# Kernel optimization log

Measured on AMD Instinct MI355X. Metric: run time of the kernel, lower is better.

The kernel has to match this reference:

```python
import jax, jax.numpy as jnp
import numpy as np
from jax import lax

HEADS = 8
LN_EPS = 1e-5


def setup_inputs() -> dict:
    key = jax.random.key(0)
    k = jax.random.split(key, 8)
    B, C, H, W, r = 4, 64, 64, 64, 4
    T = H * W
    x = jax.random.normal(k[0], (B, C, H, W), dtype=jnp.float32)
    conv_w = jax.random.normal(k[1], (C, C, r, r), dtype=jnp.float32) * 0.02  # OIHW
    conv_b = jnp.zeros((C,), dtype=jnp.float32)
    ln_g = jnp.ones((C,), dtype=jnp.float32)
    ln_b = jnp.zeros((C,), dtype=jnp.float32)
    Wqkv = jax.random.normal(k[2], (C, 3 * C), dtype=jnp.float32) * 0.02  # to_qvk (no bias)
    W0 = jax.random.normal(k[3], (C, C), dtype=jnp.float32) * 0.02  # output proj (no bias)
    E = jax.random.normal(k[4], (T, T // 4), dtype=jnp.float32)  # Linformer proj (randn in torch fwd)
    return {"x": x, "conv_w": conv_w, "conv_b": conv_b, "ln_g": ln_g,
            "ln_b": ln_b, "Wqkv": Wqkv, "W0": W0, "E": E}


def _layernorm2d(y, g, b):
    # LayerNorm over channel dim of NCHW (torch: permute to NHWC, LN last dim)
    yt = y.transpose(0, 2, 3, 1)  # b h w c
    mu = yt.mean(-1, keepdims=True)
    var = ((yt - mu) ** 2).mean(-1, keepdims=True)
    yt = (yt - mu) * lax.rsqrt(var + LN_EPS) * g + b
    return yt.transpose(0, 3, 1, 2)


def reference(x, conv_w, conv_b, ln_g, ln_b, Wqkv, W0, E):
    B, C, H, W = x.shape
    T = H * W
    dh = C // HEADS
    r = conv_w.shape[-1]

    # reducer: conv(stride=r) + LayerNorm2d. NOTE: faithful to the torch module,
    # this result is computed but NEVER used by the output (dead code in source).
    red = lax.conv_general_dilated(x, conv_w, (r, r), 'VALID',
                                   dimension_numbers=('NCHW', 'OIHW', 'NCHW'))
    red = red + conv_b[None, :, None, None]
    _red = _layernorm2d(red, ln_g, ln_b)  # unused, matches source

    # tokens from full-resolution x: b c h w -> b (h w) c
    xf = x.reshape(B, C, T).transpose(0, 2, 1)  # [B,T,C]
    qkv = xf @ Wqkv  # [B,T,3C]
    # rearrange 'b t (d k h)' with k=3, h=HEADS -> composite order (d, k, h)
    qkv = qkv.reshape(B, T, dh, 3, HEADS)
    q = qkv[:, :, :, 0, :].transpose(0, 3, 1, 2)  # [B,h,T,d]
    kk = qkv[:, :, :, 1, :].transpose(0, 3, 1, 2)
    v = qkv[:, :, :, 2, :].transpose(0, 3, 1, 2)

    # Linformer low-rank projection of V and K: [B,h,T,d] x [T,k] -> [B,h,k,d]
    v = jnp.einsum('bhjd,jk->bhkd', v, E)
    kk = jnp.einsum('bhjd,jk->bhkd', kk, E)

    scale = dh ** -0.5
    scores = jnp.einsum('bhid,bhjd->bhij', q, kk) * scale  # [B,h,T,k]
    attn = jax.nn.softmax(scores, axis=-1)
    out = jnp.einsum('bhij,bhjd->bhid', attn, v)  # [B,h,T,d]

    out = out.transpose(0, 2, 1, 3).reshape(B, T, C)  # b h i d -> b i (h d)
    out = out @ W0  # [B,T,C]
    return out.transpose(0, 2, 1).reshape(B, C, H, W)
```

## Files before the change

kernel.cpp:

```cpp
#include <hip/hip_runtime.h>

#define T_DIM 4096
#define KD    1024
#define SCALE 0.35355339059327373f

typedef __attribute__((ext_vector_type(8))) short bf16x8;
typedef __attribute__((ext_vector_type(4))) short bf16x4;
typedef __attribute__((ext_vector_type(4))) float f32x4;

__device__ inline unsigned cvt_pk_bf16(float a, float b) {
  unsigned ua = __float_as_uint(a); ua += 0x7fffu + ((ua >> 16) & 1u);
  unsigned ub = __float_as_uint(b); ub += 0x7fffu + ((ub >> 16) & 1u);
  return (ua >> 16) | (ub & 0xffff0000u);
}

__device__ inline bf16x4 mk4(unsigned lo, unsigned hi) {
  union { unsigned u[2]; bf16x4 v; } x; x.u[0] = lo; x.u[1] = hi; return x.v;
}

__device__ inline bf16x8 mk8(unsigned a, unsigned b, unsigned c, unsigned d) {
  union { unsigned u[4]; bf16x8 v; } x;
  x.u[0] = a; x.u[1] = b; x.u[2] = c; x.u[3] = d; return x.v;
}

__device__ inline f32x4 mfma16(bf16x4 a, bf16x4 b, f32x4 c) {
  bf16x8 a8 = {}, b8 = {};
  a8[0] = a[0]; a8[1] = a[1]; a8[2] = a[2]; a8[3] = a[3];
  b8[0] = b[0]; b8[1] = b[1]; b8[2] = b[2]; b8[3] = b[3];
  return __builtin_amdgcn_mfma_f32_16x16x32_bf16(a8, b8, c, 0, 0, 0);
}

__global__ __launch_bounds__(256) void k_q(const float* __restrict__ x,
                                           const float* __restrict__ Wqkv,
                                           float* __restrict__ Q) {
  const int g  = blockIdx.x;
  const int tt = blockIdx.y;
  const int b  = blockIdx.z;
  const int t  = tt * 256 + threadIdx.x;
  const int col0 = g * 24;

  float acc[8];
#pragma unroll
  for (int j = 0; j < 8; ++j) acc[j] = 0.f;

  const float* xb = x + (size_t)b * 64 * T_DIM + t;
#pragma unroll 4
  for (int c = 0; c < 64; ++c) {
    float xv = xb[(size_t)c * T_DIM];
    const float* wr = Wqkv + c * 192 + col0;
#pragma unroll
    for (int h = 0; h < 8; ++h) acc[h] += xv * wr[h];
  }
#pragma unroll
  for (int h = 0; h < 8; ++h)
    Q[(((size_t)(b * 8 + h)) * 8 + g) * T_DIM + t] = acc[h];
}

__global__ __launch_bounds__(256) void k_xe(const float* __restrict__ x,
                                            const float* __restrict__ E,
                                            float* __restrict__ partial) {
  __shared__ unsigned short As[64 * 72];
  const int kb = blockIdx.x;
  const int b  = blockIdx.y;
  const int s  = blockIdx.z;
  const int k0 = kb * 128;
  const int tid = threadIdx.x;
  const int lane = tid & 63;
  const int w = tid >> 6;
  const int li = lane & 15, lg = lane >> 4;

  f32x4 acc[4][2] = {};

  const int ar = tid >> 4;
  const int af = tid & 15;

  for (int tb = 0; tb < 4; ++tb) {
    const int t0 = s * 256 + tb * 64;
    float4 av[4];
#pragma unroll
    for (int ii = 0; ii < 4; ++ii)
      av[ii] = *(const float4*)(x + ((size_t)b * 64 + ar + ii * 16) * T_DIM + t0 + af * 4);
    __syncthreads();
#pragma unroll
    for (int ii = 0; ii < 4; ++ii) {
      unsigned lo = cvt_pk_bf16(av[ii].x, av[ii].y);
      unsigned hi = cvt_pk_bf16(av[ii].z, av[ii].w);
      *(uint2*)(As + (ar + ii * 16) * 72 + af * 4) = make_uint2(lo, hi);
    }
    __syncthreads();

#pragma unroll
    for (int ks = 0; ks < 2; ++ks) {
      const int tbase = t0 + ks * 32 + lg * 8;
      bf16x8 bq[2];
#pragma unroll
      for (int nt = 0; nt < 2; ++nt) {
        const int kcol = k0 + w * 32 + nt * 16 + li;
        float bv[8];
#pragma unroll
        for (int j = 0; j < 8; ++j)
          bv[j] = E[(size_t)(tbase + j) * KD + kcol];
        bq[nt] = mk8(cvt_pk_bf16(bv[0], bv[1]), cvt_pk_bf16(bv[2], bv[3]),
                     cvt_pk_bf16(bv[4], bv[5]), cvt_pk_bf16(bv[6], bv[7]));
      }
#pragma unroll
      for (int mt = 0; mt < 4; ++mt) {
        bf16x8 af8 = *(const bf16x8*)(As + (mt * 16 + li) * 72 + ks * 32 + lg * 8);
#pragma unroll
        for (int nt = 0; nt < 2; ++nt)
          acc[mt][nt] = __builtin_amdgcn_mfma_f32_16x16x32_bf16(af8, bq[nt], acc[mt][nt], 0, 0, 0);
      }
    }
  }

  float* pb = partial + ((size_t)s * 4 + b) * (64 * KD);
#pragma unroll
  for (int mt = 0; mt < 4; ++mt)
#pragma unroll
    for (int nt = 0; nt < 2; ++nt) {
      const int row = mt * 16 + lg * 4;
      const int col = k0 + w * 32 + nt * 16 + li;
#pragma unroll
      for (int reg = 0; reg < 4; ++reg)
        pb[(size_t)(row + reg) * KD + col] = acc[mt][nt][reg];
    }
}

__global__ __launch_bounds__(256) void k_xered(const float* __restrict__ partial,
                                               unsigned short* __restrict__ XP) {
  const size_t o = ((size_t)blockIdx.x * 256 + threadIdx.x) * 4;
  const int k4 = (int)(o & 1023);
  const int cb = (int)(o >> 10);
  const size_t src = (size_t)cb * KD + k4;
  float4 a = make_float4(0.f, 0.f, 0.f, 0.f);
#pragma unroll
  for (int s = 0; s < 16; ++s) {
    float4 v = *(const float4*)(partial + ((size_t)s * 4) * (64 * KD) + src);
    a.x += v.x; a.y += v.y; a.z += v.z; a.w += v.w;
  }
  *(uint2*)(XP + o) = make_uint2(cvt_pk_bf16(a.x, a.y), cvt_pk_bf16(a.z, a.w));
}

__global__ __launch_bounds__(256) void k_kvp(const unsigned short* __restrict__ XP,
                                             const float* __restrict__ Wqkv,
                                             float* __restrict__ KVP) {
  const int kb  = blockIdx.x >> 1;
  const int sel = blockIdx.x & 1;
  const int h   = blockIdx.y;
  const int b   = blockIdx.z;
  const int k   = kb * 256 + threadIdx.x;

  float acc[8];
#pragma unroll
  for (int d = 0; d < 8; ++d) acc[d] = 0.f;

  const unsigned short* xb = XP + (size_t)b * 64 * KD + k;
#pragma unroll 4
  for (int c = 0; c < 64; ++c) {
    float xv = __uint_as_float((unsigned)xb[(size_t)c * KD] << 16);
    const float* wr = Wqkv + c * 192 + (sel + 1) * 8 + h;
#pragma unroll
    for (int d = 0; d < 8; ++d) acc[d] += xv * wr[d * 24];
  }

  float* op = KVP + (((size_t)(b * 8 + h)) * KD + k) * 16 + sel * 8;
  *(float4*)(op)     = make_float4(acc[0], acc[1], acc[2], acc[3]);
  *(float4*)(op + 4) = make_float4(acc[4], acc[5], acc[6], acc[7]);
}

#define VT_PITCH 1032
__global__ __launch_bounds__(256) void k_attn(const float* __restrict__ Q,
                                              const float* __restrict__ KVP,
                                              float* __restrict__ O) {
  __shared__ unsigned short Kt[2 * 1024 * 4];
  __shared__ unsigned short Vt[9 * VT_PITCH];
  const int bh = blockIdx.x;
  const int tid = threadIdx.x;
  const float ks = SCALE;

#pragma unroll
  for (int it = 0; it < 4; ++it) {
    const int j = it * 256 + tid;
    const float* row = KVP + ((size_t)bh * 1024 + j) * 16;
    float4 k0 = *(const float4*)(row);
    float4 k1 = *(const float4*)(row + 4);
    float4 v0 = *(const float4*)(row + 8);
    float4 v1 = *(const float4*)(row + 12);
    unsigned a0 = cvt_pk_bf16(k0.x * ks, k0.y * ks);
    unsigned a1 = cvt_pk_bf16(k0.z * ks, k0.w * ks);
    unsigned a2 = cvt_pk_bf16(k1.x * ks, k1.y * ks);
    unsigned a3 = cvt_pk_bf16(k1.z * ks, k1.w * ks);
    *(uint2*)(&Kt[(size_t)j * 4])          = make_uint2(a0, a1);
    *(uint2*)(&Kt[(size_t)(1024 + j) * 4]) = make_uint2(a2, a3);
    unsigned b0 = cvt_pk_bf16(v0.x, v0.y);
    unsigned b1 = cvt_pk_bf16(v0.z, v0.w);
    unsigned b2 = cvt_pk_bf16(v1.x, v1.y);
    unsigned b3 = cvt_pk_bf16(v1.z, v1.w);
    Vt[0 * VT_PITCH + j] = (unsigned short)b0;
    Vt[1 * VT_PITCH + j] = (unsigned short)(b0 >> 16);
    Vt[2 * VT_PITCH + j] = (unsigned short)b1;
    Vt[3 * VT_PITCH + j] = (unsigned short)(b1 >> 16);
    Vt[4 * VT_PITCH + j] = (unsigned short)b2;
    Vt[5 * VT_PITCH + j] = (unsigned short)(b2 >> 16);
    Vt[6 * VT_PITCH + j] = (unsigned short)b3;
    Vt[7 * VT_PITCH + j] = (unsigned short)(b3 >> 16);
    Vt[8 * VT_PITCH + j] = 0x3F80;
  }
  __syncthreads();

  const int lane = tid & 63, w = tid >> 6;
  const int li = lane & 15, lg = lane >> 4;
  const int i0w = blockIdx.y * 128 + w * 32;

  bf16x4 qf[2] = {bf16x4{}, bf16x4{}};
  if (lane < 32) {
#pragma unroll
    for (int it2 = 0; it2 < 2; ++it2) {
      const float* qp = Q + ((size_t)bh * 8 + lg * 4) * T_DIM + i0w + it2 * 16 + li;
      qf[it2] = mk4(cvt_pk_bf16(qp[0], qp[T_DIM]),
                    cvt_pk_bf16(qp[2 * T_DIM], qp[3 * T_DIM]));
    }
  }

  f32x4 accO[2] = {f32x4{0.f, 0.f, 0.f, 0.f}, f32x4{0.f, 0.f, 0.f, 0.f}};
#pragma unroll 2
  for (int jt = 0; jt < 1024; jt += 16) {
    bf16x4 kf = {};
    if (lane < 32) kf = *(const bf16x4*)(&Kt[(size_t)(lg * 1024 + jt + li) * 4]);
    bf16x4 vf = {};
    if (li < 9) vf = *(const bf16x4*)(&Vt[li * VT_PITCH + jt + lg * 4]);
#pragma unroll
    for (int it2 = 0; it2 < 2; ++it2) {
      f32x4 st = mfma16(kf, qf[it2], f32x4{0.f, 0.f, 0.f, 0.f});
      f32x4 p;
      p[0] = __expf(st[0]); p[1] = __expf(st[1]);
      p[2] = __expf(st[2]); p[3] = __expf(st[3]);
      bf16x4 pf = mk4(cvt_pk_bf16(p[0], p[1]), cvt_pk_bf16(p[2], p[3]));
      accO[it2] = mfma16(vf, pf, accO[it2]);
    }
  }

  const int b = bh >> 3, h = bh & 7;
#pragma unroll
  for (int it2 = 0; it2 < 2; ++it2) {
    float l = __shfl(accO[it2][0], 32 + li);
    float inv = 1.0f / l;
    if (lane < 32) {
      const int i = i0w + it2 * 16 + li;
      float4 o = make_float4(accO[it2][0] * inv, accO[it2][1] * inv,
                             accO[it2][2] * inv, accO[it2][3] * inv);
      *(float4*)(O + ((size_t)b * T_DIM + i) * 64 + h * 8 + lg * 4) = o;
    }
  }
}

__global__ __launch_bounds__(256) void k_out(const float* __restrict__ O,
                                             const float* __restrict__ W0,
                                             float* __restrict__ out) {
  const int cg = blockIdx.x;
  const int tt = blockIdx.y;
  const int b  = blockIdx.z;
  const int t  = tt * 256 + threadIdx.x;
  const int col0 = cg * 8;

  float acc[8];
#pragma unroll
  for (int j = 0; j < 8; ++j) acc[j] = 0.f;

  const float* orow = O + ((size_t)b * T_DIM + t) * 64;
#pragma unroll
  for (int c0 = 0; c0 < 64; c0 += 4) {
    float4 v = *(const float4*)(orow + c0);
    float ov[4] = {v.x, v.y, v.z, v.w};
#pragma unroll
    for (int u = 0; u < 4; ++u) {
      const float* wr = W0 + (c0 + u) * 64 + col0;
#pragma unroll
      for (int j = 0; j < 8; ++j) acc[j] += ov[u] * wr[j];
    }
  }
#pragma unroll
  for (int j = 0; j < 8; ++j)
    out[((size_t)b * 64 + col0 + j) * T_DIM + t] = acc[j];
}

extern "C" void kernel_launch(void* const* d_in, const int* in_sizes, int n_in,
                              void* d_out, int out_size, void* d_ws, size_t ws_size,
                              hipStream_t stream) {
  const float* x    = (const float*)d_in[0];
  const float* Wqkv = (const float*)d_in[5];
  const float* W0   = (const float*)d_in[6];
  const float* E    = (const float*)d_in[7];
  float* out = (float*)d_out;

  float* Q       = (float*)d_ws;
  float* O       = Q + 1048576;
  float* KVP     = O + 1048576;
  float* partial = KVP + 524288;
  unsigned short* XP = (unsigned short*)(partial + 4194304);

  k_q     <<<dim3(8, 16, 4), 256, 0, stream>>>(x, Wqkv, Q);
  k_xe    <<<dim3(8, 4, 16), 256, 0, stream>>>(x, E, partial);
  k_xered <<<dim3(256),      256, 0, stream>>>(partial + (size_t)0, XP);
  k_kvp   <<<dim3(8, 8, 4),  256, 0, stream>>>(XP, Wqkv, KVP);
  k_attn  <<<dim3(32, 32),   256, 0, stream>>>(Q, KVP, O);
  k_out   <<<dim3(8, 16, 4), 256, 0, stream>>>(O, W0, out);
}
```

Baseline: 167.9 us.

## Precompute scaled bf16 K/V layouts in k_kvp and drop LDS staging in k_xe

k_kvp now writes K already scaled and packed as bf16 in the layout the attention kernel's shared memory expects, and V as transposed bf16 rows. k_attn therefore only copies these into LDS, with no fp32 loads or per-block conversion. This matters because each of the 32 blocks per head previously re-read and re-converted the same fp32 KVP. k_xe also drops its shared-memory staging of x and its barriers, loading x fragments straight from global into MFMA operands, which trades fewer syncs for more redundant global reads across waves.

```diff
diff --git a/kernel.cpp b/kernel.cpp
--- a/kernel.cpp
+++ b/kernel.cpp
@@ -7,6 +7,12 @@
 typedef __attribute__((ext_vector_type(8))) short bf16x8;
 typedef __attribute__((ext_vector_type(4))) short bf16x4;
 typedef __attribute__((ext_vector_type(4))) float f32x4;
+
+__device__ inline unsigned short f2bf(float f) {
+  unsigned u = __float_as_uint(f);
+  unsigned r = u + 0x7fffu + ((u >> 16) & 1u);
+  return (unsigned short)(r >> 16);
+}
 
 __device__ inline unsigned cvt_pk_bf16(float a, float b) {
   unsigned ua = __float_as_uint(a); ua += 0x7fffu + ((ua >> 16) & 1u);
@@ -59,7 +65,6 @@
 __global__ __launch_bounds__(256) void k_xe(const float* __restrict__ x,
                                             const float* __restrict__ E,
                                             float* __restrict__ partial) {
-  __shared__ unsigned short As[64 * 72];
   const int kb = blockIdx.x;
   const int b  = blockIdx.y;
   const int s  = blockIdx.z;
@@ -71,45 +76,29 @@
 
   f32x4 acc[4][2] = {};
 
-  const int ar = tid >> 4;
-  const int af = tid & 15;
-
-  for (int tb = 0; tb < 4; ++tb) {
-    const int t0 = s * 256 + tb * 64;
-    float4 av[4];
-#pragma unroll
-    for (int ii = 0; ii < 4; ++ii)
-      av[ii] = *(const float4*)(x + ((size_t)b * 64 + ar + ii * 16) * T_DIM + t0 + af * 4);
-    __syncthreads();
-#pragma unroll
-    for (int ii = 0; ii < 4; ++ii) {
-      unsigned lo = cvt_pk_bf16(av[ii].x, av[ii].y);
-      unsigned hi = cvt_pk_bf16(av[ii].z, av[ii].w);
-      *(uint2*)(As + (ar + ii * 16) * 72 + af * 4) = make_uint2(lo, hi);
-    }
-    __syncthreads();
-
-#pragma unroll
-    for (int ks = 0; ks < 2; ++ks) {
-      const int tbase = t0 + ks * 32 + lg * 8;
-      bf16x8 bq[2];
-#pragma unroll
-      for (int nt = 0; nt < 2; ++nt) {
-        const int kcol = k0 + w * 32 + nt * 16 + li;
-        float bv[8];
-#pragma unroll
-        for (int j = 0; j < 8; ++j)
-          bv[j] = E[(size_t)(tbase + j) * KD + kcol];
-        bq[nt] = mk8(cvt_pk_bf16(bv[0], bv[1]), cvt_pk_bf16(bv[2], bv[3]),
-                     cvt_pk_bf16(bv[4], bv[5]), cvt_pk_bf16(bv[6], bv[7]));
-      }
-#pragma unroll
-      for (int mt = 0; mt < 4; ++mt) {
-        bf16x8 af8 = *(const bf16x8*)(As + (mt * 16 + li) * 72 + ks * 32 + lg * 8);
-#pragma unroll
-        for (int nt = 0; nt < 2; ++nt)
-          acc[mt][nt] = __builtin_amdgcn_mfma_f32_16x16x32_bf16(af8, bq[nt], acc[mt][nt], 0, 0, 0);
-      }
+#pragma unroll 2
+  for (int tb = 0; tb < 8; ++tb) {
+    const int tbase = s * 256 + tb * 32 + lg * 8;
+    bf16x8 bq[2];
+#pragma unroll
+    for (int nt = 0; nt < 2; ++nt) {
+      const int kcol = k0 + w * 32 + nt * 16 + li;
+      float bv[8];
+#pragma unroll
+      for (int j = 0; j < 8; ++j)
+        bv[j] = E[(size_t)(tbase + j) * KD + kcol];
+      bq[nt] = mk8(cvt_pk_bf16(bv[0], bv[1]), cvt_pk_bf16(bv[2], bv[3]),
+                   cvt_pk_bf16(bv[4], bv[5]), cvt_pk_bf16(bv[6], bv[7]));
+    }
+#pragma unroll
+    for (int mt = 0; mt < 4; ++mt) {
+      const float* ap = x + ((size_t)b * 64 + mt * 16 + li) * T_DIM + tbase;
+      float4 a0 = *(const float4*)(ap);
+      float4 a1 = *(const float4*)(ap + 4);
+      bf16x8 af8 = mk8(cvt_pk_bf16(a0.x, a0.y), cvt_pk_bf16(a0.z, a0.w),
+                       cvt_pk_bf16(a1.x, a1.y), cvt_pk_bf16(a1.z, a1.w));
+      acc[mt][0] = __builtin_amdgcn_mfma_f32_16x16x32_bf16(af8, bq[0], acc[mt][0], 0, 0, 0);
+      acc[mt][1] = __builtin_amdgcn_mfma_f32_16x16x32_bf16(af8, bq[1], acc[mt][1], 0, 0, 0);
     }
   }
 
@@ -143,12 +132,13 @@
 
 __global__ __launch_bounds__(256) void k_kvp(const unsigned short* __restrict__ XP,
                                              const float* __restrict__ Wqkv,
-                                             float* __restrict__ KVP) {
-  const int kb  = blockIdx.x >> 1;
-  const int sel = blockIdx.x & 1;
+                                             uint2* __restrict__ Kg,
+                                             unsigned short* __restrict__ Vg) {
+  const int kb  = blockIdx.x;
   const int h   = blockIdx.y;
   const int b   = blockIdx.z;
-  const int k   = kb * 256 + threadIdx.x;
+  const int sel = threadIdx.x >> 7;
+  const int k   = kb * 128 + (threadIdx.x & 127);
 
   float acc[8];
 #pragma unroll
@@ -163,49 +153,47 @@
     for (int d = 0; d < 8; ++d) acc[d] += xv * wr[d * 24];
   }
 
-  float* op = KVP + (((size_t)(b * 8 + h)) * KD + k) * 16 + sel * 8;
-  *(float4*)(op)     = make_float4(acc[0], acc[1], acc[2], acc[3]);
-  *(float4*)(op + 4) = make_float4(acc[4], acc[5], acc[6], acc[7]);
+  const int bh = b * 8 + h;
+  if (sel == 0) {
+    uint2* kg = Kg + (size_t)bh * 2048;
+    kg[k] = make_uint2(cvt_pk_bf16(acc[0] * SCALE, acc[1] * SCALE),
+                       cvt_pk_bf16(acc[2] * SCALE, acc[3] * SCALE));
+    kg[1024 + k] = make_uint2(cvt_pk_bf16(acc[4] * SCALE, acc[5] * SCALE),
+                              cvt_pk_bf16(acc[6] * SCALE, acc[7] * SCALE));
+  } else {
+#pragma unroll
+    for (int d = 0; d < 8; ++d)
+      Vg[(size_t)(bh * 8 + d) * KD + k] = f2bf(acc[d]);
+  }
 }
 
 #define VT_PITCH 1032
 __global__ __launch_bounds__(256) void k_attn(const float* __restrict__ Q,
-                                              const float* __restrict__ KVP,
+                                              const uint2* __restrict__ Kg,
+                                              const unsigned short* __restrict__ Vg,
                                               float* __restrict__ O) {
   __shared__ unsigned short Kt[2 * 1024 * 4];
   __shared__ unsigned short Vt[9 * VT_PITCH];
   const int bh = blockIdx.x;
   const int tid = threadIdx.x;
-  const float ks = SCALE;
-
-#pragma unroll
-  for (int it = 0; it < 4; ++it) {
-    const int j = it * 256 + tid;
-    const float* row = KVP + ((size_t)bh * 1024 + j) * 16;
-    float4 k0 = *(const float4*)(row);
-    float4 k1 = *(const float4*)(row + 4);
-    float4 v0 = *(const float4*)(row + 8);
-    float4 v1 = *(const float4*)(row + 12);
-    unsigned a0 = cvt_pk_bf16(k0.x * ks, k0.y * ks);
-    unsigned a1 = cvt_pk_bf16(k0.z * ks, k0.w * ks);
-    unsigned a2 = cvt_pk_bf16(k1.x * ks, k1.y * ks);
-    unsigned a3 = cvt_pk_bf16(k1.z * ks, k1.w * ks);
-    *(uint2*)(&Kt[(size_t)j * 4])          = make_uint2(a0, a1);
-    *(uint2*)(&Kt[(size_t)(1024 + j) * 4]) = make_uint2(a2, a3);
-    unsigned b0 = cvt_pk_bf16(v0.x, v0.y);
-    unsigned b1 = cvt_pk_bf16(v0.z, v0.w);
-    unsigned b2 = cvt_pk_bf16(v1.x, v1.y);
-    unsigned b3 = cvt_pk_bf16(v1.z, v1.w);
-    Vt[0 * VT_PITCH + j] = (unsigned short)b0;
-    Vt[1 * VT_PITCH + j] = (unsigned short)(b0 >> 16);
-    Vt[2 * VT_PITCH + j] = (unsigned short)b1;
-    Vt[3 * VT_PITCH + j] = (unsigned short)(b1 >> 16);
-    Vt[4 * VT_PITCH + j] = (unsigned short)b2;
-    Vt[5 * VT_PITCH + j] = (unsigned short)(b2 >> 16);
-    Vt[6 * VT_PITCH + j] = (unsigned short)b3;
-    Vt[7 * VT_PITCH + j] = (unsigned short)(b3 >> 16);
-    Vt[8 * VT_PITCH + j] = 0x3F80;
-  }
+
+  const uint2* kg = Kg + (size_t)bh * 2048;
+  uint2* kt2 = (uint2*)Kt;
+#pragma unroll
+  for (int it = 0; it < 8; ++it)
+    kt2[it * 256 + tid] = kg[it * 256 + tid];
+  const unsigned* vg = (const unsigned*)(Vg + (size_t)bh * 8192);
+#pragma unroll
+  for (int dd = 0; dd < 8; ++dd) {
+#pragma unroll
+    for (int it = 0; it < 2; ++it) {
+      const int j2 = it * 256 + tid;
+      *(unsigned*)(Vt + dd * VT_PITCH + j2 * 2) = vg[dd * 512 + j2];
+    }
+  }
+#pragma unroll
+  for (int it = 0; it < 2; ++it)
+    *(unsigned*)(Vt + 8 * VT_PITCH + (it * 256 + tid) * 2) = 0x3F803F80u;
   __syncthreads();
 
   const int lane = tid & 63, w = tid >> 6;
@@ -295,14 +283,15 @@
 
   float* Q       = (float*)d_ws;
   float* O       = Q + 1048576;
-  float* KVP     = O + 1048576;
-  float* partial = KVP + 524288;
+  float* partial = O + 1048576;
   unsigned short* XP = (unsigned short*)(partial + 4194304);
+  uint2* Kg          = (uint2*)(XP + 262144);
+  unsigned short* Vg = (unsigned short*)(Kg + 65536);
 
   k_q     <<<dim3(8, 16, 4), 256, 0, stream>>>(x, Wqkv, Q);
   k_xe    <<<dim3(8, 4, 16), 256, 0, stream>>>(x, E, partial);
-  k_xered <<<dim3(256),      256, 0, stream>>>(partial + (size_t)0, XP);
-  k_kvp   <<<dim3(8, 8, 4),  256, 0, stream>>>(XP, Wqkv, KVP);
-  k_attn  <<<dim3(32, 32),   256, 0, stream>>>(Q, KVP, O);
+  k_xered <<<dim3(256),      256, 0, stream>>>(partial, XP);
+  k_kvp   <<<dim3(8, 8, 4),  256, 0, stream>>>(XP, Wqkv, Kg, Vg);
+  k_attn  <<<dim3(32, 32),   256, 0, stream>>>(Q, Kg, Vg, O);
   k_out   <<<dim3(8, 16, 4), 256, 0, stream>>>(O, W0, out);
 }
```

Measured after the change: 169.8 us. About the same (+1.1%).
